# Kernel tuning notes

Hardware: AMD Instinct MI355X
Metric: run time of the kernel (lower is better)

## Reference

```python
import jax, jax.numpy as jnp
import numpy as np

N_NODES = 50000
N_EDGES = 800000
NODE_DIM = 10
EDGE_DIM = 5
HID = 64


def _tconv(x, src, dst, e_attr, wq, bq, wk, bk, wv, bv, we, ws, bs):
    # PyG TransformerConv, heads=1, concat=True, root_weight=True, beta=False
    n = x.shape[0]
    q = x @ wq + bq                      # [N, HID]
    k = x @ wk + bk                      # [N, HID]
    v = x @ wv + bv                      # [N, HID]
    ee = e_attr @ we                     # [E, HID] (lin_edge, no bias)
    ke = k[src] + ee                     # key per edge
    ve = v[src] + ee                     # value per edge
    logits = jnp.sum(q[dst] * ke, axis=-1) / 8.0  # sqrt(64) = 8
    m = jax.ops.segment_max(logits, dst, num_segments=n)
    p = jnp.exp(logits - m[dst])
    s = jax.ops.segment_sum(p, dst, num_segments=n)
    alpha = p / s[dst]                   # segment softmax over in-neighbors
    agg = jax.ops.segment_sum(alpha[:, None] * ve, dst, num_segments=n)
    return agg + x @ ws + bs             # + lin_skip(x_i)


def setup_inputs() -> dict:
    key = jax.random.key(0)
    ks = jax.random.split(key, 32)
    x = jax.random.uniform(ks[0], (N_NODES, NODE_DIM), dtype=jnp.float32)
    edge_index = jax.random.randint(ks[1], (2, N_EDGES), 0, N_NODES, dtype=jnp.int64)
    edge_attr = jax.random.uniform(ks[2], (N_EDGES, EDGE_DIM), dtype=jnp.float32)

    def lin(k, fan_in, fan_out):
        b = 1.0 / np.sqrt(fan_in)
        return jax.random.uniform(k, (fan_in, fan_out), jnp.float32, -b, b)

    def bias(k, fan_in, fan_out):
        b = 1.0 / np.sqrt(fan_in)
        return jax.random.uniform(k, (fan_out,), jnp.float32, -b, b)

    inp = dict(x=x, edge_index=edge_index, edge_attr=edge_attr)
    # conv1: NODE_DIM -> HID
    inp['w1q'] = lin(ks[3], NODE_DIM, HID); inp['b1q'] = bias(ks[4], NODE_DIM, HID)
    inp['w1k'] = lin(ks[5], NODE_DIM, HID); inp['b1k'] = bias(ks[6], NODE_DIM, HID)
    inp['w1v'] = lin(ks[7], NODE_DIM, HID); inp['b1v'] = bias(ks[8], NODE_DIM, HID)
    inp['w1e'] = lin(ks[9], EDGE_DIM, HID)
    inp['w1s'] = lin(ks[10], NODE_DIM, HID); inp['b1s'] = bias(ks[11], NODE_DIM, HID)
    # 5 stacked HID -> HID layers
    inp['wq'] = jnp.stack([lin(jax.random.fold_in(ks[12], i), HID, HID) for i in range(5)])
    inp['bq'] = jnp.stack([bias(jax.random.fold_in(ks[13], i), HID, HID) for i in range(5)])
    inp['wk'] = jnp.stack([lin(jax.random.fold_in(ks[14], i), HID, HID) for i in range(5)])
    inp['bk'] = jnp.stack([bias(jax.random.fold_in(ks[15], i), HID, HID) for i in range(5)])
    inp['wv'] = jnp.stack([lin(jax.random.fold_in(ks[16], i), HID, HID) for i in range(5)])
    inp['bv'] = jnp.stack([bias(jax.random.fold_in(ks[17], i), HID, HID) for i in range(5)])
    inp['we'] = jnp.stack([lin(jax.random.fold_in(ks[18], i), EDGE_DIM, HID) for i in range(5)])
    inp['ws'] = jnp.stack([lin(jax.random.fold_in(ks[19], i), HID, HID) for i in range(5)])
    inp['bs'] = jnp.stack([bias(jax.random.fold_in(ks[20], i), HID, HID) for i in range(5)])
    # final linear HID -> 1
    inp['lin_w'] = lin(ks[21], HID, 1); inp['lin_b'] = bias(ks[22], HID, 1)
    return inp


def reference(x, edge_index, edge_attr, w1q, b1q, w1k, b1k, w1v, b1v, w1e, w1s, b1s,
              wq, bq, wk, bk, wv, bv, we, ws, bs, lin_w, lin_b):
    src, dst = edge_index[0], edge_index[1]  # x_j = x[src], aggregated into dst
    h = jnp.log(x + 1.0)
    e = jnp.log(edge_attr + 1.0)
    h = _tconv(h, src, dst, e, w1q, b1q, w1k, b1k, w1v, b1v, w1e, w1s, b1s)
    for i in range(5):
        h = _tconv(h, src, dst, e, wq[i], bq[i], wk[i], bk[i], wv[i], bv[i], we[i], ws[i], bs[i])
    return h @ lin_w + lin_b  # [N, 1]
```

## Files before the change

### kernel.cpp

```cpp
#include <hip/hip_runtime.h>
#include <hip/hip_fp16.h>
#include <cstdint>
#include <cstddef>

#define NN 50000
#define NE 800000
#define HD 64
#define SB 49
#define NT64 6250

__global__ void k_hist(const int* __restrict__ ei, int* __restrict__ cnt) {
    int e = blockIdx.x * blockDim.x + threadIdx.x;
    if (e < NE) atomicAdd(&cnt[ei[NE + e]], 1);
}

__global__ __launch_bounds__(256) void k_scan1(const int* __restrict__ cnt,
                                               int* __restrict__ row_start,
                                               int* __restrict__ bsum) {
    __shared__ int ssum[256];
    const int tid = threadIdx.x, b = blockIdx.x;
    const int i0 = b * 1024 + tid * 4;
    int c0 = 0, c1 = 0, c2 = 0, c3 = 0;
    if (i0 + 3 < NN) {
        const int4 c = *(const int4*)(cnt + i0);
        c0 = c.x; c1 = c.y; c2 = c.z; c3 = c.w;
    } else {
        if (i0 + 0 < NN) c0 = cnt[i0 + 0];
        if (i0 + 1 < NN) c1 = cnt[i0 + 1];
        if (i0 + 2 < NN) c2 = cnt[i0 + 2];
        if (i0 + 3 < NN) c3 = cnt[i0 + 3];
    }
    ssum[tid] = c0 + c1 + c2 + c3;
    __syncthreads();
    for (int off = 1; off < 256; off <<= 1) {
        int v = (tid >= off) ? ssum[tid - off] : 0;
        __syncthreads();
        ssum[tid] += v;
        __syncthreads();
    }
    int ex = (tid == 0) ? 0 : ssum[tid - 1];
    if (i0 + 0 < NN) row_start[i0 + 0] = ex;
    ex += c0;
    if (i0 + 1 < NN) row_start[i0 + 1] = ex;
    ex += c1;
    if (i0 + 2 < NN) row_start[i0 + 2] = ex;
    ex += c2;
    if (i0 + 3 < NN) row_start[i0 + 3] = ex;
    if (tid == 255) bsum[b] = ssum[255];
}

__global__ __launch_bounds__(64) void k_scan2(const int* __restrict__ bsum,
                                              int* __restrict__ boff,
                                              int* __restrict__ row_start) {
    __shared__ int s[64];
    const int t = threadIdx.x;
    s[t] = (t < SB) ? bsum[t] : 0;
    __syncthreads();
    for (int off = 1; off < 64; off <<= 1) {
        int v = (t >= off) ? s[t - off] : 0;
        __syncthreads();
        s[t] += v;
        __syncthreads();
    }
    if (t < SB) boff[t] = (t == 0) ? 0 : s[t - 1];
    if (t == 0) row_start[NN] = s[SB - 1];
}

__global__ __launch_bounds__(256) void k_scan3(int* __restrict__ row_start,
                                               const int* __restrict__ boff,
                                               int* __restrict__ cur) {
    const int b = blockIdx.x;
    const int i0 = b * 1024 + threadIdx.x * 4;
    const int o = boff[b];
#pragma unroll
    for (int k = 0; k < 4; ++k) {
        int i = i0 + k;
        if (i < NN) {
            int v = row_start[i] + o;
            row_start[i] = v;
            cur[i] = v;
        }
    }
}

__global__ void k_scatter(const int* __restrict__ ei, const float* __restrict__ ea,
                          int* __restrict__ cur, uint4* __restrict__ e5p) {
    int e = blockIdx.x * blockDim.x + threadIdx.x;
    if (e < NE) {
        int d = ei[NE + e];
        int pos = atomicAdd(&cur[d], 1);
        const float e0 = __logf(ea[(size_t)e * 5 + 0] + 1.f);
        const float e1 = __logf(ea[(size_t)e * 5 + 1] + 1.f);
        const float e2 = __logf(ea[(size_t)e * 5 + 2] + 1.f);
        const float e3 = __logf(ea[(size_t)e * 5 + 3] + 1.f);
        const float e4 = __logf(ea[(size_t)e * 5 + 4] + 1.f);
        union { __half2 h; unsigned u; } c01, c23;
        c01.h = __floats2half2_rn(e0, e1);
        c23.h = __floats2half2_rn(e2, e3);
        uint4 rec;
        rec.x = c01.u;
        rec.y = c23.u;
        rec.z = ((unsigned)ei[e] << 16) |
                (unsigned)__half_as_ushort(__float2half_rn(e4));
        rec.w = 0u;
        e5p[pos] = rec;
    }
}

__device__ __forceinline__ void cvt_kv(const uint4 u, float4& k4, float4& v4) {
    const float2 p0 = __half22float2(*(const __half2*)&u.x);
    const float2 p1 = __half22float2(*(const __half2*)&u.y);
    const float2 p2 = __half22float2(*(const __half2*)&u.z);
    const float2 p3 = __half22float2(*(const __half2*)&u.w);
    k4 = make_float4(p0.x, p1.x, p2.x, p3.x);
    v4 = make_float4(p0.y, p1.y, p2.y, p3.y);
}

__global__ __launch_bounds__(256, 4) void k_qkvs64(
    const float* __restrict__ h,
    const float* __restrict__ Wq, const float* __restrict__ Bq,
    const float* __restrict__ Wk, const float* __restrict__ Bk,
    const float* __restrict__ Wv, const float* __restrict__ Bv,
    const float* __restrict__ Ws, const float* __restrict__ Bs,
    float* __restrict__ qb, __half* __restrict__ kvh, float* __restrict__ sb) {
    __shared__ float xs[2][512];
    __shared__ float kls[512];
    const int lane = threadIdx.x & 63;
    const int w = threadIdx.x >> 6;
    const float* W = (w == 0) ? Wq : (w == 1) ? Ws : (w == 2) ? Wk : Wv;
    const float* B = (w == 0) ? Bq : (w == 1) ? Bs : (w == 2) ? Bk : Bv;
    const float scl = (w == 0) ? 0.125f : 1.f;
    float wr[64];
#pragma unroll
    for (int j = 0; j < 64; ++j) wr[j] = W[j * 64 + lane] * scl;
    const float bias = B[lane] * scl;

    int tile = blockIdx.x;
    {
        const float2 g = *(const float2*)(h + (size_t)tile * 512 + threadIdx.x * 2);
        *(float2*)&xs[0][threadIdx.x * 2] = g;
    }
    __syncthreads();
    int buf = 0;
    while (true) {
        const int nt = tile + gridDim.x;
        const bool more = nt < NT64;
        float2 gn;
        if (more) gn = *(const float2*)(h + (size_t)nt * 512 + threadIdx.x * 2);
        float acc[8] = {bias, bias, bias, bias, bias, bias, bias, bias};
#pragma unroll
        for (int jq = 0; jq < 16; ++jq) {
#pragma unroll
            for (int n = 0; n < 8; ++n) {
                const float4 xv = *(const float4*)&xs[buf][n * 64 + jq * 4];
                acc[n] = fmaf(xv.x, wr[jq * 4 + 0], acc[n]);
                acc[n] = fmaf(xv.y, wr[jq * 4 + 1], acc[n]);
                acc[n] = fmaf(xv.z, wr[jq * 4 + 2], acc[n]);
                acc[n] = fmaf(xv.w, wr[jq * 4 + 3], acc[n]);
            }
        }
        if (w == 2) {
#pragma unroll
            for (int n = 0; n < 8; ++n) kls[n * 64 + lane] = acc[n];
        }
        if (more) *(float2*)&xs[buf ^ 1][threadIdx.x * 2] = gn;
        __syncthreads();
        const int nb = tile * 8;
        if (w == 0) {
#pragma unroll
            for (int n = 0; n < 8; ++n) qb[(size_t)(nb + n) * 64 + lane] = acc[n];
        } else if (w == 1) {
#pragma unroll
            for (int n = 0; n < 8; ++n) sb[(size_t)(nb + n) * 64 + lane] = acc[n];
        } else if (w == 3) {
#pragma unroll
            for (int n = 0; n < 8; ++n) {
                const float kk = kls[n * 64 + lane];
                *(__half2*)(kvh + (size_t)(nb + n) * 128 + lane * 2) =
                    __floats2half2_rn(kk, acc[n]);
            }
        }
        if (!more) break;
        __syncthreads();
        tile = nt;
        buf ^= 1;
    }
}

__global__ __launch_bounds__(256, 4) void k_qkvs10(
    const float* __restrict__ x,
    const float* __restrict__ Wq, const float* __restrict__ Bq,
    const float* __restrict__ Wk, const float* __restrict__ Bk,
    const float* __restrict__ Wv, const float* __restrict__ Bv,
    const float* __restrict__ Ws, const float* __restrict__ Bs,
    float* __restrict__ qb, __half* __restrict__ kvh, float* __restrict__ sb) {
    __shared__ float xs[640];
    const int lane = threadIdx.x & 63;
    const int w = threadIdx.x >> 6;
    const bool iskv = (w == 1 || w == 3);
    const float* WA = (w == 0) ? Wq : iskv ? Wk : Ws;
    const float* BA = (w == 0) ? Bq : iskv ? Bk : Bs;
    const float scl = (w == 0) ? 0.125f : 1.f;
    float wrA[10], wrB[10];
#pragma unroll
    for (int j = 0; j < 10; ++j) {
        wrA[j] = WA[j * 64 + lane] * scl;
        wrB[j] = iskv ? Wv[j * 64 + lane] : 0.f;
    }
    const float bA = BA[lane] * scl;
    const float bB = iskv ? Bv[lane] : 0.f;
    const int tile = blockIdx.x;
    const int fbase = tile * 640;
    const int fcnt = min(640, NN * 10 - fbase);
    if (threadIdx.x * 4 < fcnt) {
        float4 v = *(const float4*)(x + (size_t)fbase + threadIdx.x * 4);
        v.x = __logf(v.x + 1.f);
        v.y = __logf(v.y + 1.f);
        v.z = __logf(v.z + 1.f);
        v.w = __logf(v.w + 1.f);
        *(float4*)&xs[threadIdx.x * 4] = v;
    }
    __syncthreads();
    const int nbase = tile * 64;
    const int nodes = min(64, NN - nbase);
    const int n0 = (w == 3) ? 32 : 0;
    const int n1 = iskv ? ((w == 1) ? min(nodes, 32) : nodes) : nodes;
    for (int n = n0; n < n1; ++n) {
        float accA = bA, accB = bB;
#pragma unroll
        for (int j = 0; j < 10; ++j) {
            const float xv = xs[n * 10 + j];
            accA = fmaf(xv, wrA[j], accA);
            accB = fmaf(xv, wrB[j], accB);
        }
        const size_t node = (size_t)(nbase + n);
        if (iskv) {
            const __half2 hv = __floats2half2_rn(accA, accB);
            *(__half2*)(kvh + node * 128 + lane * 2) = hv;
        } else if (w == 0) {
            qb[node * 64 + lane] = accA;
        } else {
            sb[node * 64 + lane] = accA;
        }
    }
}

template <bool FINAL>
__global__ __launch_bounds__(256) void k_agg(
    const float* __restrict__ q, const __half* __restrict__ kv,
    const float* __restrict__ sk, const uint4* __restrict__ e5p,
    const float* __restrict__ wE, const int* __restrict__ row_start,
    float* __restrict__ hout, const float* __restrict__ lw, const float* lb) {
    const int lane = threadIdx.x & 63;
    const int g = lane >> 4, t = lane & 15;
    const int node = __builtin_amdgcn_readfirstlane(blockIdx.x * 4 + (threadIdx.x >> 6));
    if (node >= NN) return;
    const int beg = row_start[node], end = row_start[node + 1];
    if (beg == end) {
        const float4 s4 = *(const float4*)(sk + (size_t)node * 64 + t * 4);
        if (FINAL) {
            const float4 lw4 = *(const float4*)(lw + t * 4);
            float r = s4.x * lw4.x;
            r = fmaf(s4.y, lw4.y, r);
            r = fmaf(s4.z, lw4.z, r);
            r = fmaf(s4.w, lw4.w, r);
            r += __shfl_xor(r, 1);
            r += __shfl_xor(r, 2);
            r += __shfl_xor(r, 4);
            r += __shfl_xor(r, 8);
            if (lane == 0) hout[node] = r + lb[0];
        } else if (g == 0) {
            *(float4*)(hout + (size_t)node * 64 + t * 4) = s4;
        }
        return;
    }
    const float4 q4 = *(const float4*)(q + (size_t)node * 64 + t * 4);
    float g5[5];
    {
        const float4 wg = *(const float4*)(wE + g * 64 + t * 4);
        float dc = q4.x * wg.x;
        dc = fmaf(q4.y, wg.y, dc);
        dc = fmaf(q4.z, wg.z, dc);
        dc = fmaf(q4.w, wg.w, dc);
        dc += __shfl_xor(dc, 1);
        dc += __shfl_xor(dc, 2);
        dc += __shfl_xor(dc, 4);
        dc += __shfl_xor(dc, 8);
        const float4 w4 = *(const float4*)(wE + 4 * 64 + t * 4);
        float d4 = q4.x * w4.x;
        d4 = fmaf(q4.y, w4.y, d4);
        d4 = fmaf(q4.z, w4.z, d4);
        d4 = fmaf(q4.w, w4.w, d4);
        d4 += __shfl_xor(d4, 1);
        d4 += __shfl_xor(d4, 2);
        d4 += __shfl_xor(d4, 4);
        d4 += __shfl_xor(d4, 8);
        g5[0] = __shfl(dc, 0);
        g5[1] = __shfl(dc, 16);
        g5[2] = __shfl(dc, 32);
        g5[3] = __shfl(dc, 48);
        g5[4] = __shfl(d4, 0);
    }
    float m = -1e30f, l = 0.f;
    float4 accv = {0.f, 0.f, 0.f, 0.f};
    float a50 = 0.f, a51 = 0.f, a52 = 0.f, a53 = 0.f, a54 = 0.f;
    const char* kvc = (const char*)kv;
    const int i0x = beg + g;
    const int i0 = (i0x < end) ? i0x : beg;
    uint4 r0 = e5p[i0];
    const int i1x = beg + 4 + g;
    const int i1 = (i1x < end) ? i1x : beg;
    uint4 r1 = e5p[i1];
    uint4 kv8 =
        *(const uint4*)(kvc + (size_t)((r0.z & 0xffff0000u) >> 8) + t * 16);
#pragma unroll 2
    for (int p = beg; p < end; p += 4) {
        const int nx = p + 8 + g;
        const int npp = (nx < end) ? nx : beg;
        const uint4 rn = e5p[npp];
        const uint4 nkv =
            *(const uint4*)(kvc + (size_t)((r1.z & 0xffff0000u) >> 8) + t * 16);
        const bool act = (p + g) < end;
        float4 k4, v4;
        cvt_kv(kv8, k4, v4);
        const float2 e01 = __half22float2(*(const __half2*)&r0.x);
        const float2 e23 = __half22float2(*(const __half2*)&r0.y);
        const float e4v =
            __half2float(__ushort_as_half((unsigned short)(r0.z & 0xffffu)));
        float d = q4.x * k4.x;
        d = fmaf(q4.y, k4.y, d);
        d = fmaf(q4.z, k4.z, d);
        d = fmaf(q4.w, k4.w, d);
        d += __shfl_xor(d, 1);
        d += __shfl_xor(d, 2);
        d += __shfl_xor(d, 4);
        d += __shfl_xor(d, 8);
        float d5 = g5[0] * e01.x;
        d5 = fmaf(g5[1], e01.y, d5);
        d5 = fmaf(g5[2], e23.x, d5);
        d5 = fmaf(g5[3], e23.y, d5);
        d5 = fmaf(g5[4], e4v, d5);
        const float la = act ? (d + d5) : -__builtin_inff();
        float pa = __expf(la - m);
        if (la > m + 8.f) {
            const float rs = __expf(m - la);
            l *= rs;
            accv.x *= rs;
            accv.y *= rs;
            accv.z *= rs;
            accv.w *= rs;
            a50 *= rs;
            a51 *= rs;
            a52 *= rs;
            a53 *= rs;
            a54 *= rs;
            m = la;
            pa = 1.f;
        }
        l += pa;
        accv.x = fmaf(pa, v4.x, accv.x);
        accv.y = fmaf(pa, v4.y, accv.y);
        accv.z = fmaf(pa, v4.z, accv.z);
        accv.w = fmaf(pa, v4.w, accv.w);
        a50 = fmaf(pa, e01.x, a50);
        a51 = fmaf(pa, e01.y, a51);
        a52 = fmaf(pa, e23.x, a52);
        a53 = fmaf(pa, e23.y, a53);
        a54 = fmaf(pa, e4v, a54);
        r0 = r1;
        r1 = rn;
        kv8 = nkv;
    }
    float M = fmaxf(m, __shfl_xor(m, 16));
    M = fmaxf(M, __shfl_xor(M, 32));
    const float f = __expf(m - M);
    float lz = l * f;
    lz += __shfl_xor(lz, 16);
    lz += __shfl_xor(lz, 32);
    accv.x *= f;
    accv.y *= f;
    accv.z *= f;
    accv.w *= f;
    a50 *= f;
    a51 *= f;
    a52 *= f;
    a53 *= f;
    a54 *= f;
#pragma unroll
    for (int s = 16; s <= 32; s <<= 1) {
        accv.x += __shfl_xor(accv.x, s);
        accv.y += __shfl_xor(accv.y, s);
        accv.z += __shfl_xor(accv.z, s);
        accv.w += __shfl_xor(accv.w, s);
        a50 += __shfl_xor(a50, s);
        a51 += __shfl_xor(a51, s);
        a52 += __shfl_xor(a52, s);
        a53 += __shfl_xor(a53, s);
        a54 += __shfl_xor(a54, s);
    }
    float4 t4 = accv;
    {
        const float4 w0 = *(const float4*)(wE + 0 * 64 + t * 4);
        const float4 w1 = *(const float4*)(wE + 1 * 64 + t * 4);
        const float4 w2 = *(const float4*)(wE + 2 * 64 + t * 4);
        const float4 w3 = *(const float4*)(wE + 3 * 64 + t * 4);
        const float4 w4r = *(const float4*)(wE + 4 * 64 + t * 4);
        t4.x = fmaf(a50, w0.x, t4.x);
        t4.y = fmaf(a50, w0.y, t4.y);
        t4.z = fmaf(a50, w0.z, t4.z);
        t4.w = fmaf(a50, w0.w, t4.w);
        t4.x = fmaf(a51, w1.x, t4.x);
        t4.y = fmaf(a51, w1.y, t4.y);
        t4.z = fmaf(a51, w1.z, t4.z);
        t4.w = fmaf(a51, w1.w, t4.w);
        t4.x = fmaf(a52, w2.x, t4.x);
        t4.y = fmaf(a52, w2.y, t4.y);
        t4.z = fmaf(a52, w2.z, t4.z);
        t4.w = fmaf(a52, w2.w, t4.w);
        t4.x = fmaf(a53, w3.x, t4.x);
        t4.y = fmaf(a53, w3.y, t4.y);
        t4.z = fmaf(a53, w3.z, t4.z);
        t4.w = fmaf(a53, w3.w, t4.w);
        t4.x = fmaf(a54, w4r.x, t4.x);
        t4.y = fmaf(a54, w4r.y, t4.y);
        t4.z = fmaf(a54, w4r.z, t4.z);
        t4.w = fmaf(a54, w4r.w, t4.w);
    }
    const float4 s4 = *(const float4*)(sk + (size_t)node * 64 + t * 4);
    const float rl = 1.f / lz;
    float4 o;
    o.x = fmaf(t4.x, rl, s4.x);
    o.y = fmaf(t4.y, rl, s4.y);
    o.z = fmaf(t4.z, rl, s4.z);
    o.w = fmaf(t4.w, rl, s4.w);
    if (FINAL) {
        const float4 lw4 = *(const float4*)(lw + t * 4);
        float r = o.x * lw4.x;
        r = fmaf(o.y, lw4.y, r);
        r = fmaf(o.z, lw4.z, r);
        r = fmaf(o.w, lw4.w, r);
        r += __shfl_xor(r, 1);
        r += __shfl_xor(r, 2);
        r += __shfl_xor(r, 4);
        r += __shfl_xor(r, 8);
        if (lane == 0) hout[node] = r + lb[0];
    } else if (g == 0) {
        *(float4*)(hout + (size_t)node * 64 + t * 4) = o;
    }
}

extern "C" void kernel_launch(void* const* d_in, const int* in_sizes, int n_in,
                              void* d_out, int out_size, void* d_ws, size_t ws_size,
                              hipStream_t stream) {
    const float* x = (const float*)d_in[0];
    const int* ei = (const int*)d_in[1];
    const float* ea = (const float*)d_in[2];
    const float* w1q = (const float*)d_in[3];
    const float* b1q = (const float*)d_in[4];
    const float* w1k = (const float*)d_in[5];
    const float* b1k = (const float*)d_in[6];
    const float* w1v = (const float*)d_in[7];
    const float* b1v = (const float*)d_in[8];
    const float* w1e = (const float*)d_in[9];
    const float* w1s = (const float*)d_in[10];
    const float* b1s = (const float*)d_in[11];
    const float* wq = (const float*)d_in[12];
    const float* bq = (const float*)d_in[13];
    const float* wk = (const float*)d_in[14];
    const float* bk = (const float*)d_in[15];
    const float* wv = (const float*)d_in[16];
    const float* bv = (const float*)d_in[17];
    const float* we = (const float*)d_in[18];
    const float* ws = (const float*)d_in[19];
    const float* bs = (const float*)d_in[20];
    const float* lw = (const float*)d_in[21];
    const float* lb = (const float*)d_in[22];

    uintptr_t p = (uintptr_t)d_ws;
    auto alloc = [&](size_t bytes) -> void* {
        void* r = (void*)p;
        p += (bytes + 255) & ~(size_t)255;
        return r;
    };
    uint4* e5p = (uint4*)alloc((size_t)NE * 16);
    float* hb = (float*)alloc((size_t)NN * HD * 4);
    __half* kvh = (__half*)alloc((size_t)NN * 128 * 2);
    float* qb = (float*)alloc((size_t)NN * HD * 4);
    float* sb = (float*)alloc((size_t)NN * HD * 4);
    int* row_start = (int*)alloc((size_t)(NN + 1) * 4);
    int* cnt = (int*)alloc((size_t)NN * 4);
    int* cur = (int*)alloc((size_t)NN * 4);
    int* bsum = (int*)alloc((size_t)SB * 4);
    int* boff = (int*)alloc((size_t)SB * 4);

    hipMemsetAsync(cnt, 0, (size_t)NN * 4, stream);
    k_hist<<<(NE + 255) / 256, 256, 0, stream>>>(ei, cnt);
    k_scan1<<<SB, 256, 0, stream>>>(cnt, row_start, bsum);
    k_scan2<<<1, 64, 0, stream>>>(bsum, boff, row_start);
    k_scan3<<<SB, 256, 0, stream>>>(row_start, boff, cur);
    k_scatter<<<(NE + 255) / 256, 256, 0, stream>>>(ei, ea, cur, e5p);

    const int gg64 = 1024;
    const int gg10 = (NN + 63) / 64;
    const int agg_grid = (NN + 3) / 4;

    k_qkvs10<<<gg10, 256, 0, stream>>>(x, w1q, b1q, w1k, b1k, w1v, b1v, w1s, b1s,
                                       qb, kvh, sb);
    k_agg<false><<<agg_grid, 256, 0, stream>>>(qb, kvh, sb, e5p, w1e, row_start,
                                               hb, lw, lb);

    for (int i = 0; i < 5; ++i) {
        k_qkvs64<<<gg64, 256, 0, stream>>>(hb, wq + i * 4096, bq + i * 64,
                                           wk + i * 4096, bk + i * 64,
                                           wv + i * 4096, bv + i * 64,
                                           ws + i * 4096, bs + i * 64,
                                           qb, kvh, sb);
        if (i < 4) {
            k_agg<false><<<agg_grid, 256, 0, stream>>>(qb, kvh, sb, e5p,
                                                       we + i * 320, row_start, hb,
                                                       lw, lb);
        } else {
            k_agg<true><<<agg_grid, 256, 0, stream>>>(qb, kvh, sb, e5p,
                                                      we + i * 320, row_start,
                                                      (float*)d_out, lw, lb);
        }
    }
}
```

Measured before the change: 616.0 us.

## Fuse next-layer QKVS projection into aggregation kernel epilogue

After: 620.9 us. Within noise of the previous version (+0.8%).

```diff
diff --git a/kernel.cpp b/kernel.cpp
--- a/kernel.cpp
+++ b/kernel.cpp
@@ -7,7 +7,6 @@
 #define NE 800000
 #define HD 64
 #define SB 49
-#define NT64 6250
 
 __global__ void k_hist(const int* __restrict__ ei, int* __restrict__ cnt) {
     int e = blockIdx.x * blockDim.x + threadIdx.x;
@@ -116,77 +115,6 @@
     v4 = make_float4(p0.y, p1.y, p2.y, p3.y);
 }
 
-__global__ __launch_bounds__(256, 4) void k_qkvs64(
-    const float* __restrict__ h,
-    const float* __restrict__ Wq, const float* __restrict__ Bq,
-    const float* __restrict__ Wk, const float* __restrict__ Bk,
-    const float* __restrict__ Wv, const float* __restrict__ Bv,
-    const float* __restrict__ Ws, const float* __restrict__ Bs,
-    float* __restrict__ qb, __half* __restrict__ kvh, float* __restrict__ sb) {
-    __shared__ float xs[2][512];
-    __shared__ float kls[512];
-    const int lane = threadIdx.x & 63;
-    const int w = threadIdx.x >> 6;
-    const float* W = (w == 0) ? Wq : (w == 1) ? Ws : (w == 2) ? Wk : Wv;
-    const float* B = (w == 0) ? Bq : (w == 1) ? Bs : (w == 2) ? Bk : Bv;
-    const float scl = (w == 0) ? 0.125f : 1.f;
-    float wr[64];
-#pragma unroll
-    for (int j = 0; j < 64; ++j) wr[j] = W[j * 64 + lane] * scl;
-    const float bias = B[lane] * scl;
-
-    int tile = blockIdx.x;
-    {
-        const float2 g = *(const float2*)(h + (size_t)tile * 512 + threadIdx.x * 2);
-        *(float2*)&xs[0][threadIdx.x * 2] = g;
-    }
-    __syncthreads();
-    int buf = 0;
-    while (true) {
-        const int nt = tile + gridDim.x;
-        const bool more = nt < NT64;
-        float2 gn;
-        if (more) gn = *(const float2*)(h + (size_t)nt * 512 + threadIdx.x * 2);
-        float acc[8] = {bias, bias, bias, bias, bias, bias, bias, bias};
-#pragma unroll
-        for (int jq = 0; jq < 16; ++jq) {
-#pragma unroll
-            for (int n = 0; n < 8; ++n) {
-                const float4 xv = *(const float4*)&xs[buf][n * 64 + jq * 4];
-                acc[n] = fmaf(xv.x, wr[jq * 4 + 0], acc[n]);
-                acc[n] = fmaf(xv.y, wr[jq * 4 + 1], acc[n]);
-                acc[n] = fmaf(xv.z, wr[jq * 4 + 2], acc[n]);
-                acc[n] = fmaf(xv.w, wr[jq * 4 + 3], acc[n]);
-            }
-        }
-        if (w == 2) {
-#pragma unroll
-            for (int n = 0; n < 8; ++n) kls[n * 64 + lane] = acc[n];
-        }
-        if (more) *(float2*)&xs[buf ^ 1][threadIdx.x * 2] = gn;
-        __syncthreads();
-        const int nb = tile * 8;
-        if (w == 0) {
-#pragma unroll
-            for (int n = 0; n < 8; ++n) qb[(size_t)(nb + n) * 64 + lane] = acc[n];
-        } else if (w == 1) {
-#pragma unroll
-            for (int n = 0; n < 8; ++n) sb[(size_t)(nb + n) * 64 + lane] = acc[n];
-        } else if (w == 3) {
-#pragma unroll
-            for (int n = 0; n < 8; ++n) {
-                const float kk = kls[n * 64 + lane];
-                *(__half2*)(kvh + (size_t)(nb + n) * 128 + lane * 2) =
-                    __floats2half2_rn(kk, acc[n]);
-            }
-        }
-        if (!more) break;
-        __syncthreads();
-        tile = nt;
-        buf ^= 1;
-    }
-}
-
 __global__ __launch_bounds__(256, 4) void k_qkvs10(
     const float* __restrict__ x,
     const float* __restrict__ Wq, const float* __restrict__ Bq,
@@ -250,202 +178,236 @@
     const float* __restrict__ q, const __half* __restrict__ kv,
     const float* __restrict__ sk, const uint4* __restrict__ e5p,
     const float* __restrict__ wE, const int* __restrict__ row_start,
-    float* __restrict__ hout, const float* __restrict__ lw, const float* lb) {
+    float* __restrict__ hout, const float* __restrict__ lw, const float* lb,
+    const float* __restrict__ Wq, const float* __restrict__ Bq,
+    const float* __restrict__ Wk, const float* __restrict__ Bk,
+    const float* __restrict__ Wv, const float* __restrict__ Bv,
+    const float* __restrict__ Ws, const float* __restrict__ Bs,
+    float* __restrict__ qout, __half* __restrict__ kvout,
+    float* __restrict__ sout) {
+    __shared__ float ols[256];
+    __shared__ float kls[256];
     const int lane = threadIdx.x & 63;
+    const int wave = threadIdx.x >> 6;
     const int g = lane >> 4, t = lane & 15;
-    const int node = __builtin_amdgcn_readfirstlane(blockIdx.x * 4 + (threadIdx.x >> 6));
-    if (node >= NN) return;
+    const int node = __builtin_amdgcn_readfirstlane(blockIdx.x * 4 + wave);
     const int beg = row_start[node], end = row_start[node + 1];
+    const float4 s4 = *(const float4*)(sk + (size_t)node * 64 + t * 4);
+    float4 o4;
     if (beg == end) {
-        const float4 s4 = *(const float4*)(sk + (size_t)node * 64 + t * 4);
-        if (FINAL) {
-            const float4 lw4 = *(const float4*)(lw + t * 4);
-            float r = s4.x * lw4.x;
-            r = fmaf(s4.y, lw4.y, r);
-            r = fmaf(s4.z, lw4.z, r);
-            r = fmaf(s4.w, lw4.w, r);
-            r += __shfl_xor(r, 1);
-            r += __shfl_xor(r, 2);
-            r += __shfl_xor(r, 4);
-            r += __shfl_xor(r, 8);
-            if (lane == 0) hout[node] = r + lb[0];
-        } else if (g == 0) {
-            *(float4*)(hout + (size_t)node * 64 + t * 4) = s4;
-        }
-        return;
-    }
-    const float4 q4 = *(const float4*)(q + (size_t)node * 64 + t * 4);
-    float g5[5];
-    {
-        const float4 wg = *(const float4*)(wE + g * 64 + t * 4);
-        float dc = q4.x * wg.x;
-        dc = fmaf(q4.y, wg.y, dc);
-        dc = fmaf(q4.z, wg.z, dc);
-        dc = fmaf(q4.w, wg.w, dc);
-        dc += __shfl_xor(dc, 1);
-        dc += __shfl_xor(dc, 2);
-        dc += __shfl_xor(dc, 4);
-        dc += __shfl_xor(dc, 8);
-        const float4 w4 = *(const float4*)(wE + 4 * 64 + t * 4);
-        float d4 = q4.x * w4.x;
-        d4 = fmaf(q4.y, w4.y, d4);
-        d4 = fmaf(q4.z, w4.z, d4);
-        d4 = fmaf(q4.w, w4.w, d4);
-        d4 += __shfl_xor(d4, 1);
-        d4 += __shfl_xor(d4, 2);
-        d4 += __shfl_xor(d4, 4);
-        d4 += __shfl_xor(d4, 8);
-        g5[0] = __shfl(dc, 0);
-        g5[1] = __shfl(dc, 16);
-        g5[2] = __shfl(dc, 32);
-        g5[3] = __shfl(dc, 48);
-        g5[4] = __shfl(d4, 0);
-    }
-    float m = -1e30f, l = 0.f;
-    float4 accv = {0.f, 0.f, 0.f, 0.f};
-    float a50 = 0.f, a51 = 0.f, a52 = 0.f, a53 = 0.f, a54 = 0.f;
-    const char* kvc = (const char*)kv;
-    const int i0x = beg + g;
-    const int i0 = (i0x < end) ? i0x : beg;
-    uint4 r0 = e5p[i0];
-    const int i1x = beg + 4 + g;
-    const int i1 = (i1x < end) ? i1x : beg;
-    uint4 r1 = e5p[i1];
-    uint4 kv8 =
-        *(const uint4*)(kvc + (size_t)((r0.z & 0xffff0000u) >> 8) + t * 16);
+        o4 = s4;
+    } else {
+        const float4 q4 = *(const float4*)(q + (size_t)node * 64 + t * 4);
+        float g5[5];
+        {
+            const float4 wg = *(const float4*)(wE + g * 64 + t * 4);
+            float dc = q4.x * wg.x;
+            dc = fmaf(q4.y, wg.y, dc);
+            dc = fmaf(q4.z, wg.z, dc);
+            dc = fmaf(q4.w, wg.w, dc);
+            dc += __shfl_xor(dc, 1);
+            dc += __shfl_xor(dc, 2);
+            dc += __shfl_xor(dc, 4);
+            dc += __shfl_xor(dc, 8);
+            const float4 w4 = *(const float4*)(wE + 4 * 64 + t * 4);
+            float d4 = q4.x * w4.x;
+            d4 = fmaf(q4.y, w4.y, d4);
+            d4 = fmaf(q4.z, w4.z, d4);
+            d4 = fmaf(q4.w, w4.w, d4);
+            d4 += __shfl_xor(d4, 1);
+            d4 += __shfl_xor(d4, 2);
+            d4 += __shfl_xor(d4, 4);
+            d4 += __shfl_xor(d4, 8);
+            g5[0] = __shfl(dc, 0);
+            g5[1] = __shfl(dc, 16);
+            g5[2] = __shfl(dc, 32);
+            g5[3] = __shfl(dc, 48);
+            g5[4] = __shfl(d4, 0);
+        }
+        float m = -1e30f, l = 0.f;
+        float4 accv = {0.f, 0.f, 0.f, 0.f};
+        float a50 = 0.f, a51 = 0.f, a52 = 0.f, a53 = 0.f, a54 = 0.f;
+        const char* kvc = (const char*)kv;
+        const int i0x = beg + g;
+        const int i0 = (i0x < end) ? i0x : beg;
+        uint4 r0 = e5p[i0];
+        const int i1x = beg + 4 + g;
+        const int i1 = (i1x < end) ? i1x : beg;
+        uint4 r1 = e5p[i1];
+        uint4 kv8 =
+            *(const uint4*)(kvc + (size_t)((r0.z & 0xffff0000u) >> 8) + t * 16);
 #pragma unroll 2
-    for (int p = beg; p < end; p += 4) {
-        const int nx = p + 8 + g;
-        const int npp = (nx < end) ? nx : beg;
-        const uint4 rn = e5p[npp];
-        const uint4 nkv =
-            *(const uint4*)(kvc + (size_t)((r1.z & 0xffff0000u) >> 8) + t * 16);
-        const bool act = (p + g) < end;
-        float4 k4, v4;
-        cvt_kv(kv8, k4, v4);
-        const float2 e01 = __half22float2(*(const __half2*)&r0.x);
-        const float2 e23 = __half22float2(*(const __half2*)&r0.y);
-        const float e4v =
-            __half2float(__ushort_as_half((unsigned short)(r0.z & 0xffffu)));
-        float d = q4.x * k4.x;
-        d = fmaf(q4.y, k4.y, d);
-        d = fmaf(q4.z, k4.z, d);
-        d = fmaf(q4.w, k4.w, d);
-        d += __shfl_xor(d, 1);
-        d += __shfl_xor(d, 2);
-        d += __shfl_xor(d, 4);
-        d += __shfl_xor(d, 8);
-        float d5 = g5[0] * e01.x;
-        d5 = fmaf(g5[1], e01.y, d5);
-        d5 = fmaf(g5[2], e23.x, d5);
-        d5 = fmaf(g5[3], e23.y, d5);
-        d5 = fmaf(g5[4], e4v, d5);
-        const float la = act ? (d + d5) : -__builtin_inff();
-        float pa = __expf(la - m);
-        if (la > m + 8.f) {
-            const float rs = __expf(m - la);
-            l *= rs;
-            accv.x *= rs;
-            accv.y *= rs;
-            accv.z *= rs;
-            accv.w *= rs;
-            a50 *= rs;
-            a51 *= rs;
-            a52 *= rs;
-            a53 *= rs;
-            a54 *= rs;
-            m = la;
-            pa = 1.f;
-        }
-        l += pa;
-        accv.x = fmaf(pa, v4.x, accv.x);
-        accv.y = fmaf(pa, v4.y, accv.y);
-        accv.z = fmaf(pa, v4.z, accv.z);
-        accv.w = fmaf(pa, v4.w, accv.w);
-        a50 = fmaf(pa, e01.x, a50);
-        a51 = fmaf(pa, e01.y, a51);
-        a52 = fmaf(pa, e23.x, a52);
-        a53 = fmaf(pa, e23.y, a53);
-        a54 = fmaf(pa, e4v, a54);
-        r0 = r1;
-        r1 = rn;
-        kv8 = nkv;
-    }
-    float M = fmaxf(m, __shfl_xor(m, 16));
-    M = fmaxf(M, __shfl_xor(M, 32));
-    const float f = __expf(m - M);
-    float lz = l * f;
-    lz += __shfl_xor(lz, 16);
-    lz += __shfl_xor(lz, 32);
-    accv.x *= f;
-    accv.y *= f;
-    accv.z *= f;
-    accv.w *= f;
-    a50 *= f;
-    a51 *= f;
-    a52 *= f;
-    a53 *= f;
-    a54 *= f;
-#pragma unroll
-    for (int s = 16; s <= 32; s <<= 1) {
-        accv.x += __shfl_xor(accv.x, s);
-        accv.y += __shfl_xor(accv.y, s);
-        accv.z += __shfl_xor(accv.z, s);
-        accv.w += __shfl_xor(accv.w, s);
-        a50 += __shfl_xor(a50, s);
-        a51 += __shfl_xor(a51, s);
-        a52 += __shfl_xor(a52, s);
-        a53 += __shfl_xor(a53, s);
-        a54 += __shfl_xor(a54, s);
-    }
-    float4 t4 = accv;
-    {
-        const float4 w0 = *(const float4*)(wE + 0 * 64 + t * 4);
-        const float4 w1 = *(const float4*)(wE + 1 * 64 + t * 4);
-        const float4 w2 = *(const float4*)(wE + 2 * 64 + t * 4);
-        const float4 w3 = *(const float4*)(wE + 3 * 64 + t * 4);
-        const float4 w4r = *(const float4*)(wE + 4 * 64 + t * 4);
-        t4.x = fmaf(a50, w0.x, t4.x);
-        t4.y = fmaf(a50, w0.y, t4.y);
-        t4.z = fmaf(a50, w0.z, t4.z);
-        t4.w = fmaf(a50, w0.w, t4.w);
-        t4.x = fmaf(a51, w1.x, t4.x);
-        t4.y = fmaf(a51, w1.y, t4.y);
-        t4.z = fmaf(a51, w1.z, t4.z);
-        t4.w = fmaf(a51, w1.w, t4.w);
-        t4.x = fmaf(a52, w2.x, t4.x);
-        t4.y = fmaf(a52, w2.y, t4.y);
-        t4.z = fmaf(a52, w2.z, t4.z);
-        t4.w = fmaf(a52, w2.w, t4.w);
-        t4.x = fmaf(a53, w3.x, t4.x);
-        t4.y = fmaf(a53, w3.y, t4.y);
-        t4.z = fmaf(a53, w3.z, t4.z);
-        t4.w = fmaf(a53, w3.w, t4.w);
-        t4.x = fmaf(a54, w4r.x, t4.x);
-        t4.y = fmaf(a54, w4r.y, t4.y);
-        t4.z = fmaf(a54, w4r.z, t4.z);
-        t4.w = fmaf(a54, w4r.w, t4.w);
-    }
-    const float4 s4 = *(const float4*)(sk + (size_t)node * 64 + t * 4);
-    const float rl = 1.f / lz;
-    float4 o;
-    o.x = fmaf(t4.x, rl, s4.x);
-    o.y = fmaf(t4.y, rl, s4.y);
-    o.z = fmaf(t4.z, rl, s4.z);
-    o.w = fmaf(t4.w, rl, s4.w);
+        for (int p = beg; p < end; p += 4) {
+            const int nx = p + 8 + g;
+            const int npp = (nx < end) ? nx : beg;
+            const uint4 rn = e5p[npp];
+            const uint4 nkv =
+                *(const uint4*)(kvc + (size_t)((r1.z & 0xffff0000u) >> 8) + t * 16);
+            const bool act = (p + g) < end;
+            float4 k4, v4;
+            cvt_kv(kv8, k4, v4);
+            const float2 e01 = __half22float2(*(const __half2*)&r0.x);
+            const float2 e23 = __half22float2(*(const __half2*)&r0.y);
+            const float e4v =
+                __half2float(__ushort_as_half((unsigned short)(r0.z & 0xffffu)));
+            float d = q4.x * k4.x;
+            d = fmaf(q4.y, k4.y, d);
+            d = fmaf(q4.z, k4.z, d);
+            d = fmaf(q4.w, k4.w, d);
+            d += __shfl_xor(d, 1);
+            d += __shfl_xor(d, 2);
+            d += __shfl_xor(d, 4);
+            d += __shfl_xor(d, 8);
+            float d5 = g5[0] * e01.x;
+            d5 = fmaf(g5[1], e01.y, d5);
+            d5 = fmaf(g5[2], e23.x, d5);
+            d5 = fmaf(g5[3], e23.y, d5);
+            d5 = fmaf(g5[4], e4v, d5);
+            const float la = act ? (d + d5) : -__builtin_inff();
+            float pa = __expf(la - m);
+            if (la > m + 8.f) {
+                const float rs = __expf(m - la);
+                l *= rs;
+                accv.x *= rs;
+                accv.y *= rs;
+                accv.z *= rs;
+                accv.w *= rs;
+                a50 *= rs;
+                a51 *= rs;
+                a52 *= rs;
+                a53 *= rs;
+                a54 *= rs;
+                m = la;
+                pa = 1.f;
+            }
+            l += pa;
+            accv.x = fmaf(pa, v4.x, accv.x);
+            accv.y = fmaf(pa, v4.y, accv.y);
+            accv.z = fmaf(pa, v4.z, accv.z);
+            accv.w = fmaf(pa, v4.w, accv.w);
+            a50 = fmaf(pa, e01.x, a50);
+            a51 = fmaf(pa, e01.y, a51);
+            a52 = fmaf(pa, e23.x, a52);
+            a53 = fmaf(pa, e23.y, a53);
+            a54 = fmaf(pa, e4v, a54);
+            r0 = r1;
+            r1 = rn;
+            kv8 = nkv;
+        }
+        float M = fmaxf(m, __shfl_xor(m, 16));
+        M = fmaxf(M, __shfl_xor(M, 32));
+        const float f = __expf(m - M);
+        float lz = l * f;
+        lz += __shfl_xor(lz, 16);
+        lz += __shfl_xor(lz, 32);
+        accv.x *= f;
+        accv.y *= f;
+        accv.z *= f;
+        accv.w *= f;
+        a50 *= f;
+        a51 *= f;
+        a52 *= f;
+        a53 *= f;
+        a54 *= f;
+#pragma unroll
+        for (int s = 16; s <= 32; s <<= 1) {
+            accv.x += __shfl_xor(accv.x, s);
+            accv.y += __shfl_xor(accv.y, s);
+            accv.z += __shfl_xor(accv.z, s);
+            accv.w += __shfl_xor(accv.w, s);
+            a50 += __shfl_xor(a50, s);
+            a51 += __shfl_xor(a51, s);
+            a52 += __shfl_xor(a52, s);
+            a53 += __shfl_xor(a53, s);
+            a54 += __shfl_xor(a54, s);
+        }
+        float4 t4 = accv;
+        {
+            const float4 w0 = *(const float4*)(wE + 0 * 64 + t * 4);
+            const float4 w1 = *(const float4*)(wE + 1 * 64 + t * 4);
+            const float4 w2 = *(const float4*)(wE + 2 * 64 + t * 4);
+            const float4 w3 = *(const float4*)(wE + 3 * 64 + t * 4);
+            const float4 w4r = *(const float4*)(wE + 4 * 64 + t * 4);
+            t4.x = fmaf(a50, w0.x, t4.x);
+            t4.y = fmaf(a50, w0.y, t4.y);
+            t4.z = fmaf(a50, w0.z, t4.z);
+            t4.w = fmaf(a50, w0.w, t4.w);
+            t4.x = fmaf(a51, w1.x, t4.x);
+            t4.y = fmaf(a51, w1.y, t4.y);
+            t4.z = fmaf(a51, w1.z, t4.z);
+            t4.w = fmaf(a51, w1.w, t4.w);
+            t4.x = fmaf(a52, w2.x, t4.x);
+            t4.y = fmaf(a52, w2.y, t4.y);
+            t4.z = fmaf(a52, w2.z, t4.z);
+            t4.w = fmaf(a52, w2.w, t4.w);
+            t4.x = fmaf(a53, w3.x, t4.x);
+            t4.y = fmaf(a53, w3.y, t4.y);
+            t4.z = fmaf(a53, w3.z, t4.z);
+            t4.w = fmaf(a53, w3.w, t4.w);
+            t4.x = fmaf(a54, w4r.x, t4.x);
+            t4.y = fmaf(a54, w4r.y, t4.y);
+            t4.z = fmaf(a54, w4r.z, t4.z);
+            t4.w = fmaf(a54, w4r.w, t4.w);
+        }
+        const float rl = 1.f / lz;
+        o4.x = fmaf(t4.x, rl, s4.x);
+        o4.y = fmaf(t4.y, rl, s4.y);
+        o4.z = fmaf(t4.z, rl, s4.z);
+        o4.w = fmaf(t4.w, rl, s4.w);
+    }
     if (FINAL) {
         const float4 lw4 = *(const float4*)(lw + t * 4);
-        float r = o.x * lw4.x;
-        r = fmaf(o.y, lw4.y, r);
-        r = fmaf(o.z, lw4.z, r);
-        r = fmaf(o.w, lw4.w, r);
+        float r = o4.x * lw4.x;
+        r = fmaf(o4.y, lw4.y, r);
+        r = fmaf(o4.z, lw4.z, r);
+        r = fmaf(o4.w, lw4.w, r);
         r += __shfl_xor(r, 1);
         r += __shfl_xor(r, 2);
         r += __shfl_xor(r, 4);
         r += __shfl_xor(r, 8);
         if (lane == 0) hout[node] = r + lb[0];
-    } else if (g == 0) {
-        *(float4*)(hout + (size_t)node * 64 + t * 4) = o;
+        return;
+    }
+    if (g == 0) *(float4*)&ols[wave * 64 + t * 4] = o4;
+    __syncthreads();
+    const float* W = (wave == 0) ? Wq : (wave == 1) ? Ws : (wave == 2) ? Wk : Wv;
+    const float* B = (wave == 0) ? Bq : (wave == 1) ? Bs : (wave == 2) ? Bk : Bv;
+    const float scl = (wave == 0) ? 0.125f : 1.f;
+    float wr[64];
+#pragma unroll
+    for (int j = 0; j < 64; ++j) wr[j] = W[j * 64 + lane] * scl;
+    const float bias = B[lane] * scl;
+    float acc[4] = {bias, bias, bias, bias};
+#pragma unroll
+    for (int jq = 0; jq < 16; ++jq) {
+#pragma unroll
+        for (int n = 0; n < 4; ++n) {
+            const float4 xv = *(const float4*)&ols[n * 64 + jq * 4];
+            acc[n] = fmaf(xv.x, wr[jq * 4 + 0], acc[n]);
+            acc[n] = fmaf(xv.y, wr[jq * 4 + 1], acc[n]);
+            acc[n] = fmaf(xv.z, wr[jq * 4 + 2], acc[n]);
+            acc[n] = fmaf(xv.w, wr[jq * 4 + 3], acc[n]);
+        }
+    }
+    if (wave == 2) {
+#pragma unroll
+        for (int n = 0; n < 4; ++n) kls[n * 64 + lane] = acc[n];
+    }
+    __syncthreads();
+    const int nb = blockIdx.x * 4;
+    if (wave == 0) {
+#pragma unroll
+        for (int n = 0; n < 4; ++n) qout[(size_t)(nb + n) * 64 + lane] = acc[n];
+    } else if (wave == 1) {
+#pragma unroll
+        for (int n = 0; n < 4; ++n) sout[(size_t)(nb + n) * 64 + lane] = acc[n];
+    } else if (wave == 3) {
+#pragma unroll
+        for (int n = 0; n < 4; ++n) {
+            const float kk = kls[n * 64 + lane];
+            *(__half2*)(kvout + (size_t)(nb + n) * 128 + lane * 2) =
+                __floats2half2_rn(kk, acc[n]);
+        }
     }
 }
 
@@ -483,10 +445,12 @@
         return r;
     };
     uint4* e5p = (uint4*)alloc((size_t)NE * 16);
-    float* hb = (float*)alloc((size_t)NN * HD * 4);
-    __half* kvh = (__half*)alloc((size_t)NN * 128 * 2);
-    float* qb = (float*)alloc((size_t)NN * HD * 4);
-    float* sb = (float*)alloc((size_t)NN * HD * 4);
+    float* qA = (float*)alloc((size_t)NN * HD * 4);
+    float* qB = (float*)alloc((size_t)NN * HD * 4);
+    float* sA = (float*)alloc((size_t)NN * HD * 4);
+    float* sB = (float*)alloc((size_t)NN * HD * 4);
+    __half* kvA = (__half*)alloc((size_t)NN * 128 * 2);
+    __half* kvB = (__half*)alloc((size_t)NN * 128 * 2);
     int* row_start = (int*)alloc((size_t)(NN + 1) * 4);
     int* cnt = (int*)alloc((size_t)NN * 4);
     int* cur = (int*)alloc((size_t)NN * 4);
@@ -500,29 +464,28 @@
     k_scan3<<<SB, 256, 0, stream>>>(row_start, boff, cur);
     k_scatter<<<(NE + 255) / 256, 256, 0, stream>>>(ei, ea, cur, e5p);
 
-    const int gg64 = 1024;
     const int gg10 = (NN + 63) / 64;
-    const int agg_grid = (NN + 3) / 4;
+    const int agg_grid = NN / 4;
 
     k_qkvs10<<<gg10, 256, 0, stream>>>(x, w1q, b1q, w1k, b1k, w1v, b1v, w1s, b1s,
-                                       qb, kvh, sb);
-    k_agg<false><<<agg_grid, 256, 0, stream>>>(qb, kvh, sb, e5p, w1e, row_start,
-                                               hb, lw, lb);
-
-    for (int i = 0; i < 5; ++i) {
-        k_qkvs64<<<gg64, 256, 0, stream>>>(hb, wq + i * 4096, bq + i * 64,
-                                           wk + i * 4096, bk + i * 64,
-                                           wv + i * 4096, bv + i * 64,
-                                           ws + i * 4096, bs + i * 64,
-                                           qb, kvh, sb);
-        if (i < 4) {
-            k_agg<false><<<agg_grid, 256, 0, stream>>>(qb, kvh, sb, e5p,
-                                                       we + i * 320, row_start, hb,
-                                                       lw, lb);
-        } else {
-            k_agg<true><<<agg_grid, 256, 0, stream>>>(qb, kvh, sb, e5p,
-                                                      we + i * 320, row_start,
-                                                      (float*)d_out, lw, lb);
-        }
-    }
-}
+                                       qA, kvA, sA);
+
+    const float* wEs[6] = {w1e, we, we + 320, we + 640, we + 960, we + 1280};
+    float* qin = qA;  float* qo = qB;
+    float* sin_ = sA; float* so = sB;
+    __half* kvin = kvA; __half* kvo = kvB;
+    for (int k = 0; k < 5; ++k) {
+        k_agg<false><<<agg_grid, 256, 0, stream>>>(
+            qin, kvin, sin_, e5p, wEs[k], row_start, nullptr, lw, lb,
+            wq + k * 4096, bq + k * 64, wk + k * 4096, bk + k * 64,
+            wv + k * 4096, bv + k * 64, ws + k * 4096, bs + k * 64,
+            qo, kvo, so);
+        float* tf;  __half* th;
+        tf = qin; qin = qo; qo = tf;
+        tf = sin_; sin_ = so; so = tf;
+        th = kvin; kvin = kvo; kvo = th;
+    }
+    k_agg<true><<<agg_grid, 256, 0, stream>>>(
+        qin, kvin, sin_, e5p, wEs[5], row_start, (float*)d_out, lw, lb,
+        wq, bq, wk, bk, wv, bv, ws, bs, qo, kvo, so);
+}
```
